# Performance work log

Hardware: AMD Instinct MI355X
Metric: run time of the kernel (lower is better)

## Reference

```python
import jax, jax.numpy as jnp
import numpy as np

KAPPA = 0.5


def setup_inputs() -> dict:
    key = jax.random.key(0)
    embeddings = jax.random.normal(key, (8, 4096, 64), dtype=jnp.float32)
    return {"embeddings": embeddings}


def reference(embeddings):
    # logits[b, n, m] = kappa * <emb[b,n], emb[b,m]>   -> [B, N, N]
    logits = KAPPA * jnp.einsum("bnd,bmd->bnm", embeddings, embeddings)
    B = logits.shape[0]
    # logsumexp over both matrix dims, per batch element
    loss = jax.scipy.special.logsumexp(logits.reshape(B, -1), axis=1)
    return loss.mean()
```

## Files before the change

kernel.cpp:

```cpp
#include <hip/hip_runtime.h>
#include <math.h>

#define BATCH 8
#define NTOK  4096
#define DIM   64
#define BM    128
#define NT    (NTOK / BM)
#define TPB   (NT * (NT + 1) / 2)
#define KAPPA 0.5f
#define FIXM  60.0f
#define LOG2E 1.4426950408889634f
#define C1    (KAPPA * LOG2E)
#define C2    (-FIXM * LOG2E)

typedef _Float16 f16x8  __attribute__((ext_vector_type(8)));
typedef __fp16   h2     __attribute__((ext_vector_type(2)));
typedef float    f32x16 __attribute__((ext_vector_type(16)));

__device__ __forceinline__ float exp2_fast(float x) {
#if __has_builtin(__builtin_amdgcn_exp2f)
    return __builtin_amdgcn_exp2f(x);
#else
    return __expf(x * 0.6931471805599453f);
#endif
}

__device__ __forceinline__ f16x8 pack8(float4 lo, float4 hi) {
    union { f16x8 v; h2 p[4]; } u;
    u.p[0] = __builtin_amdgcn_cvt_pkrtz(lo.x, lo.y);
    u.p[1] = __builtin_amdgcn_cvt_pkrtz(lo.z, lo.w);
    u.p[2] = __builtin_amdgcn_cvt_pkrtz(hi.x, hi.y);
    u.p[3] = __builtin_amdgcn_cvt_pkrtz(hi.z, hi.w);
    return u.v;
}

__global__ __launch_bounds__(256, 3)
void gram_lse_partial(const float* __restrict__ emb, float* __restrict__ ws) {
    __shared__ f16x8 As[8 * BM];
    __shared__ f16x8 Bs[8 * BM];

    const int tid = threadIdx.x;
    const int bb  = blockIdx.x;
    const int b   = bb / TPB;
    int t = bb - b * TPB;
    int ti = 0;
    while (t >= NT - ti) { t -= NT - ti; ++ti; }
    const int tj = ti + t;
    const bool diag = (ti == tj);

    const float* embA = emb + ((size_t)b * NTOK + (size_t)ti * BM) * DIM;
    const float* embB = emb + ((size_t)b * NTOK + (size_t)tj * BM) * DIM;

    {
        const int g  = tid & 7;
        const int r0 = tid >> 3;
#pragma unroll
        for (int p = 0; p < 4; ++p) {
            const int row = r0 + 32 * p;
            const int su  = g * BM + (row ^ g);
            const float4 a0 = *(const float4*)(embA + (size_t)row * DIM + g * 8);
            const float4 a1 = *(const float4*)(embA + (size_t)row * DIM + g * 8 + 4);
            As[su] = pack8(a0, a1);
            if (!diag) {
                const float4 b0 = *(const float4*)(embB + (size_t)row * DIM + g * 8);
                const float4 b1 = *(const float4*)(embB + (size_t)row * DIM + g * 8 + 4);
                Bs[su] = pack8(b0, b1);
            }
        }
    }
    __syncthreads();

    const int lane = tid & 63;
    const int w    = tid >> 6;
    const int half = lane >> 5;
    const int ln31 = lane & 31;
    const int waveR = (w & 1) * 64;
    const int waveC = (w >> 1) * 64;
    const f16x8* __restrict__ Bp = diag ? As : Bs;

    f32x16 acc00 = {}, acc01 = {}, acc10 = {}, acc11 = {};
#pragma unroll
    for (int s = 0; s < 4; ++s) {
        const int g = 2 * s + half;
        const f16x8 a0 = As[g * BM + ((waveR + ln31) ^ g)];
        const f16x8 a1 = As[g * BM + ((waveR + 32 + ln31) ^ g)];
        const f16x8 b0 = Bp[g * BM + ((waveC + ln31) ^ g)];
        const f16x8 b1 = Bp[g * BM + ((waveC + 32 + ln31) ^ g)];
        acc00 = __builtin_amdgcn_mfma_f32_32x32x16_f16(a0, b0, acc00, 0, 0, 0);
        acc01 = __builtin_amdgcn_mfma_f32_32x32x16_f16(a0, b1, acc01, 0, 0, 0);
        acc10 = __builtin_amdgcn_mfma_f32_32x32x16_f16(a1, b0, acc10, 0, 0, 0);
        acc11 = __builtin_amdgcn_mfma_f32_32x32x16_f16(a1, b1, acc11, 0, 0, 0);
    }

    float lsum = 0.f;
#pragma unroll
    for (int e = 0; e < 16; ++e) {
        lsum += exp2_fast(fmaf(C1, acc00[e], C2));
        lsum += exp2_fast(fmaf(C1, acc01[e], C2));
        lsum += exp2_fast(fmaf(C1, acc10[e], C2));
        lsum += exp2_fast(fmaf(C1, acc11[e], C2));
    }
#pragma unroll
    for (int off = 32; off > 0; off >>= 1)
        lsum += __shfl_xor(lsum, off);
    if (lane == 0)
        ws[4 * (size_t)bb + w] = (diag ? 1.f : 2.f) * lsum;
}

__global__ __launch_bounds__(512)
void reduce_lse(const float* __restrict__ ws, float* __restrict__ out) {
    const int tid  = threadIdx.x;
    const int w    = tid >> 6;
    const int lane = tid & 63;
    __shared__ float lse[BATCH];

    const float* p = ws + (size_t)w * TPB * 4;
    float s = 0.f;
    for (int idx = lane; idx < TPB * 4; idx += 64) s += p[idx];
#pragma unroll
    for (int off = 32; off > 0; off >>= 1) s += __shfl_xor(s, off);

    if (lane == 0) lse[w] = FIXM + logf(s);
    __syncthreads();
    if (tid == 0) {
        float a = 0.f;
        for (int i = 0; i < BATCH; ++i) a += lse[i];
        out[0] = a * (1.f / BATCH);
    }
}

extern "C" void kernel_launch(void* const* d_in, const int* in_sizes, int n_in,
                              void* d_out, int out_size, void* d_ws, size_t ws_size,
                              hipStream_t stream) {
    const float* emb = (const float*)d_in[0];
    float* out = (float*)d_out;
    float* ws  = (float*)d_ws;

    gram_lse_partial<<<BATCH * TPB, 256, 0, stream>>>(emb, ws);
    reduce_lse<<<1, 512, 0, stream>>>(ws, out);
}
```

Before: 86.58 us.

## Double tile size to 256 with 512-thread blocks and 4x2 MFMA per wave

Raises the output tile from 128x128 to 256x256 and the block size from 256 to 512 threads. Each of the 8 waves now computes a 128x64 sub-tile as 4x2 MFMA 32x32 accumulators. The load loop, workspace indexing and reduction are updated to match. Larger tiles reuse each loaded row across more outputs, so there is less global traffic and per-block overhead. The cost is fewer blocks (136×8 instead of 528×8), more LDS and registers per block, and possibly lower occupancy or worse load balance.

```diff
diff --git a/kernel.cpp b/kernel.cpp
--- a/kernel.cpp
+++ b/kernel.cpp
@@ -4,7 +4,7 @@
 #define BATCH 8
 #define NTOK  4096
 #define DIM   64
-#define BM    128
+#define BM    256
 #define NT    (NTOK / BM)
 #define TPB   (NT * (NT + 1) / 2)
 #define KAPPA 0.5f
@@ -34,7 +34,7 @@
     return u.v;
 }
 
-__global__ __launch_bounds__(256, 3)
+__global__ __launch_bounds__(512, 2)
 void gram_lse_partial(const float* __restrict__ emb, float* __restrict__ ws) {
     __shared__ f16x8 As[8 * BM];
     __shared__ f16x8 Bs[8 * BM];
@@ -56,7 +56,7 @@
         const int r0 = tid >> 3;
 #pragma unroll
         for (int p = 0; p < 4; ++p) {
-            const int row = r0 + 32 * p;
+            const int row = r0 + 64 * p;
             const int su  = g * BM + (row ^ g);
             const float4 a0 = *(const float4*)(embA + (size_t)row * DIM + g * 8);
             const float4 a1 = *(const float4*)(embA + (size_t)row * DIM + g * 8 + 4);
@@ -70,41 +70,46 @@
     }
     __syncthreads();
 
-    const int lane = tid & 63;
-    const int w    = tid >> 6;
-    const int half = lane >> 5;
-    const int ln31 = lane & 31;
-    const int waveR = (w & 1) * 64;
-    const int waveC = (w >> 1) * 64;
+    const int lane  = tid & 63;
+    const int w     = tid >> 6;
+    const int half  = lane >> 5;
+    const int ln31  = lane & 31;
+    const int rbase = (w & 1) * 128;
+    const int cbase = (w >> 1) * 64;
     const f16x8* __restrict__ Bp = diag ? As : Bs;
 
-    f32x16 acc00 = {}, acc01 = {}, acc10 = {}, acc11 = {};
+    f32x16 acc[4][2] = {};
 #pragma unroll
     for (int s = 0; s < 4; ++s) {
         const int g = 2 * s + half;
-        const f16x8 a0 = As[g * BM + ((waveR + ln31) ^ g)];
-        const f16x8 a1 = As[g * BM + ((waveR + 32 + ln31) ^ g)];
-        const f16x8 b0 = Bp[g * BM + ((waveC + ln31) ^ g)];
-        const f16x8 b1 = Bp[g * BM + ((waveC + 32 + ln31) ^ g)];
-        acc00 = __builtin_amdgcn_mfma_f32_32x32x16_f16(a0, b0, acc00, 0, 0, 0);
-        acc01 = __builtin_amdgcn_mfma_f32_32x32x16_f16(a0, b1, acc01, 0, 0, 0);
-        acc10 = __builtin_amdgcn_mfma_f32_32x32x16_f16(a1, b0, acc10, 0, 0, 0);
-        acc11 = __builtin_amdgcn_mfma_f32_32x32x16_f16(a1, b1, acc11, 0, 0, 0);
+        f16x8 af[4], bf[2];
+#pragma unroll
+        for (int i = 0; i < 4; ++i)
+            af[i] = As[g * BM + ((rbase + 32 * i + ln31) ^ g)];
+#pragma unroll
+        for (int j = 0; j < 2; ++j)
+            bf[j] = Bp[g * BM + ((cbase + 32 * j + ln31) ^ g)];
+#pragma unroll
+        for (int i = 0; i < 4; ++i)
+#pragma unroll
+            for (int j = 0; j < 2; ++j)
+                acc[i][j] = __builtin_amdgcn_mfma_f32_32x32x16_f16(
+                    af[i], bf[j], acc[i][j], 0, 0, 0);
     }
 
     float lsum = 0.f;
 #pragma unroll
-    for (int e = 0; e < 16; ++e) {
-        lsum += exp2_fast(fmaf(C1, acc00[e], C2));
-        lsum += exp2_fast(fmaf(C1, acc01[e], C2));
-        lsum += exp2_fast(fmaf(C1, acc10[e], C2));
-        lsum += exp2_fast(fmaf(C1, acc11[e], C2));
-    }
+    for (int i = 0; i < 4; ++i)
+#pragma unroll
+        for (int j = 0; j < 2; ++j)
+#pragma unroll
+            for (int e = 0; e < 16; ++e)
+                lsum += exp2_fast(fmaf(C1, acc[i][j][e], C2));
 #pragma unroll
     for (int off = 32; off > 0; off >>= 1)
         lsum += __shfl_xor(lsum, off);
     if (lane == 0)
-        ws[4 * (size_t)bb + w] = (diag ? 1.f : 2.f) * lsum;
+        ws[8 * (size_t)bb + w] = (diag ? 1.f : 2.f) * lsum;
 }
 
 __global__ __launch_bounds__(512)
@@ -114,9 +119,9 @@
     const int lane = tid & 63;
     __shared__ float lse[BATCH];
 
-    const float* p = ws + (size_t)w * TPB * 4;
+    const float* p = ws + (size_t)w * TPB * 8;
     float s = 0.f;
-    for (int idx = lane; idx < TPB * 4; idx += 64) s += p[idx];
+    for (int idx = lane; idx < TPB * 8; idx += 64) s += p[idx];
 #pragma unroll
     for (int off = 32; off > 0; off >>= 1) s += __shfl_xor(s, off);
 
@@ -136,6 +141,6 @@
     float* out = (float*)d_out;
     float* ws  = (float*)d_ws;
 
-    gram_lse_partial<<<BATCH * TPB, 256, 0, stream>>>(emb, ws);
+    gram_lse_partial<<<BATCH * TPB, 512, 0, stream>>>(emb, ws);
     reduce_lse<<<1, 512, 0, stream>>>(ws, out);
 }
```

Result: no change. 85.65 us (-1.1%).
